# Kernel optimization log

Hardware: AMD Instinct MI355X
Metric: run time of the kernel (lower is better)

The kernel has to match this reference:

```python
import jax, jax.numpy as jnp
import numpy as np

N_NODES = 100000
N_EDGES = 1600000
IN_DIM = 128
OUT_DIM = 64


def setup_inputs() -> dict:
    key = jax.random.key(0)
    k1, k2, k3, k4, k5 = jax.random.split(key, 5)
    return {
        "h_init": jax.random.normal(k1, (N_NODES, IN_DIM), dtype=jnp.float32),
        "W1": jax.random.normal(k2, (OUT_DIM, IN_DIM), dtype=jnp.float32),
        "a": jax.random.normal(k3, (1, OUT_DIM), dtype=jnp.float32),
        "src": jax.random.randint(k4, (N_EDGES,), 0, N_NODES, dtype=jnp.int64)
        if jax.config.jax_enable_x64 else jax.random.randint(k4, (N_EDGES,), 0, N_NODES, dtype=jnp.int32),
        "dst": jax.random.randint(k5, (N_EDGES,), 0, N_NODES, dtype=jnp.int32),
    }


def reference(h_init, W1, a, src, dst):
    N = h_init.shape[0]
    # node projection: [N, out_dim]
    h = h_init @ W1.T
    # per-edge diff feature: dst minus src (DGL edges.dst['h'] - edges.src['h'])
    diff = h[dst] - h[src]                       # [E, out_dim]
    e = jnp.tanh(diff @ a[0])                    # [E] edge attention logit
    # segment softmax over incoming edges of each destination node
    seg_max = jax.ops.segment_max(e, dst, num_segments=N)   # [N]
    ex = jnp.exp(e - seg_max[dst])               # [E]
    denom = jax.ops.segment_sum(ex, dst, num_segments=N)    # [N]
    alpha = ex / denom[dst]                      # [E]
    # weighted sum of diff features per destination node
    h_diff = jax.ops.segment_sum(alpha[:, None] * diff, dst, num_segments=N)  # [N, out_dim]
    return jax.nn.relu(h + h_diff)
```

## Files before the change

kernel.cpp:

```cpp
#include <hip/hip_runtime.h>
#include <hip/hip_fp16.h>

#define N_NODES 100000
#define N_EDGES 1600000
#define IN_DIM 128
#define OUT_DIM 64

#define PROJ_BLKS 782

#define NB2 782
#define MAXB2 2560
#define CUR_STRIDE 16

#define BIN_NBLK 250
#define BIN_CHUNK 6400
#define BIN_THREADS 1024

#define SG_THREADS 512

typedef short short8 __attribute__((ext_vector_type(8)));
typedef float f32x4 __attribute__((ext_vector_type(4)));

__device__ __forceinline__ short bf16_trunc(float x) {
  return (short)(__float_as_uint(x) >> 16);
}
__device__ __forceinline__ float bf16_tof(short s) {
  return __uint_as_float(((unsigned)(unsigned short)s) << 16);
}
__device__ __forceinline__ float edge_ex(float p) {
  float t2 = __expf(2.f * p);
  float th = 1.f - 2.f * __builtin_amdgcn_rcpf(t2 + 1.f);
  return __expf(th);
}

__global__ __launch_bounds__(512) void fat1_kernel(
    const float* __restrict__ h_init, const float* __restrict__ W1,
    const float* __restrict__ a, __half* __restrict__ h16,
    float* __restrict__ ha) {
  __shared__ short whi[16 * 64 * 8];
  __shared__ short wlo[16 * 64 * 8];
  int t = threadIdx.x;

  for (int idx = t; idx < 16 * 64; idx += 512) {
    int f = idx >> 6;
    int l = idx & 63;
    int kc = f >> 2, ot = f & 3;
    const float* wsrc =
        W1 + (ot * 16 + (l & 15)) * IN_DIM + kc * 32 + (l >> 4) * 8;
    short hi[8], lo[8];
#pragma unroll
    for (int j = 0; j < 8; j++) {
      float x = wsrc[j];
      short hv = bf16_trunc(x);
      hi[j] = hv;
      lo[j] = bf16_trunc(x - bf16_tof(hv));
    }
    *(short8*)&whi[idx * 8] = *(const short8*)hi;
    *(short8*)&wlo[idx * 8] = *(const short8*)lo;
  }

  int row0 = blockIdx.x * 128;
  int w = t >> 6;
  int l = t & 63;
  int m = l & 15;
  int q = l >> 4;

  int arow = row0 + w * 16 + m;
  if (arow >= N_NODES) arow = N_NODES - 1;
  const float* xsrc = h_init + (size_t)arow * IN_DIM + q * 8;

  short8 ahi[4], alo[4];
#pragma unroll
  for (int kc = 0; kc < 4; kc++) {
    float xv[8];
    *(float4*)&xv[0] = *(const float4*)(xsrc + kc * 32);
    *(float4*)&xv[4] = *(const float4*)(xsrc + kc * 32 + 4);
    short hi[8], lo[8];
#pragma unroll
    for (int j = 0; j < 8; j++) {
      short hv = bf16_trunc(xv[j]);
      hi[j] = hv;
      lo[j] = bf16_trunc(xv[j] - bf16_tof(hv));
    }
    ahi[kc] = *(const short8*)hi;
    alo[kc] = *(const short8*)lo;
  }
  __syncthreads();

  f32x4 acc[4] = {{0.f, 0.f, 0.f, 0.f},
                  {0.f, 0.f, 0.f, 0.f},
                  {0.f, 0.f, 0.f, 0.f},
                  {0.f, 0.f, 0.f, 0.f}};

#pragma unroll
  for (int kc = 0; kc < 4; kc++) {
#pragma unroll
    for (int ot = 0; ot < 4; ot++) {
      int base = (((kc << 2) | ot) * 64 + l) * 8;
      short8 bhi = *(const short8*)&whi[base];
      short8 blo = *(const short8*)&wlo[base];
      acc[ot] = __builtin_amdgcn_mfma_f32_16x16x32_bf16(ahi[kc], bhi, acc[ot],
                                                        0, 0, 0);
      acc[ot] = __builtin_amdgcn_mfma_f32_16x16x32_bf16(ahi[kc], blo, acc[ot],
                                                        0, 0, 0);
      acc[ot] = __builtin_amdgcn_mfma_f32_16x16x32_bf16(alo[kc], bhi, acc[ot],
                                                        0, 0, 0);
    }
  }

  float pa[4] = {0.f, 0.f, 0.f, 0.f};
#pragma unroll
  for (int ot = 0; ot < 4; ot++) {
    float aval = a[ot * 16 + m];
#pragma unroll
    for (int r = 0; r < 4; r++) pa[r] += acc[ot][r] * aval;
  }
  int rowb = row0 + w * 16 + q * 4;
#pragma unroll
  for (int r = 0; r < 4; r++) {
    int row = rowb + r;
    if (row < N_NODES) {
#pragma unroll
      for (int ot = 0; ot < 4; ot++)
        h16[(size_t)row * OUT_DIM + ot * 16 + m] = __float2half(acc[ot][r]);
    }
  }
#pragma unroll
  for (int r = 0; r < 4; r++) {
    pa[r] += __shfl_xor(pa[r], 1);
    pa[r] += __shfl_xor(pa[r], 2);
    pa[r] += __shfl_xor(pa[r], 4);
    pa[r] += __shfl_xor(pa[r], 8);
  }
  if (m == 0) {
#pragma unroll
    for (int r = 0; r < 4; r++) {
      int row = rowb + r;
      if (row < N_NODES) ha[row] = pa[r];
    }
  }
}

__global__ __launch_bounds__(BIN_THREADS) void bin_scatter_kernel(
    const int* __restrict__ src, const int* __restrict__ dst,
    int* __restrict__ bucket_cursor, unsigned int* __restrict__ pairs) {
  __shared__ int hst[NB2];
  __shared__ int cur[NB2];
  __shared__ int dlds[BIN_CHUNK];
  int t = threadIdx.x;
  for (int i = t; i < NB2; i += BIN_THREADS) hst[i] = 0;
  __syncthreads();
  int beg = blockIdx.x * BIN_CHUNK;
  for (int e = t; e < BIN_CHUNK; e += BIN_THREADS) {
    int d = dst[beg + e];
    dlds[e] = d;
    atomicAdd(&hst[d >> 7], 1);
  }
  __syncthreads();
  for (int i = t; i < NB2; i += BIN_THREADS) {
    int c = hst[i];
    cur[i] =
        (c > 0) ? atomicAdd(&bucket_cursor[i * CUR_STRIDE], c) + i * MAXB2 : 0;
  }
  __syncthreads();
  for (int e = t; e < BIN_CHUNK; e += BIN_THREADS) {
    int d = dlds[e];
    int pos = atomicAdd(&cur[d >> 7], 1);
    pairs[pos] = ((unsigned int)src[beg + e] << 7) | (unsigned int)(d & 127);
  }
}

__global__ __launch_bounds__(SG_THREADS) void sortgather_kernel(
    const __half* __restrict__ h16, const float* __restrict__ ha,
    const int* __restrict__ bucket_cursor,
    const unsigned int* __restrict__ pairs, float* __restrict__ out) {
  __shared__ unsigned int plds[MAXB2];
  __shared__ int2 slds[MAXB2];
  __shared__ float had[128];
  __shared__ int hist[128];
  __shared__ int scn[128];
  __shared__ int cur[128];
  __shared__ int wsum;
  int b = blockIdx.x;
  int t = threadIdx.x;
  int node0 = b << 7;
  int cnt = min(bucket_cursor[b * CUR_STRIDE], MAXB2);

  if (t < 128) {
    int node = node0 + t;
    had[t] = (node < N_NODES) ? ha[node] : 0.f;
    hist[t] = 0;
  }
  __syncthreads();
  int c4 = cnt & ~3;
  for (int i = t * 4; i < c4; i += SG_THREADS * 4) {
    uint4 p4 = *(const uint4*)&pairs[(size_t)b * MAXB2 + i];
    *(uint4*)&plds[i] = p4;
    atomicAdd(&hist[p4.x & 127u], 1);
    atomicAdd(&hist[p4.y & 127u], 1);
    atomicAdd(&hist[p4.z & 127u], 1);
    atomicAdd(&hist[p4.w & 127u], 1);
  }
  for (int i = c4 + t; i < cnt; i += SG_THREADS) {
    unsigned int p = pairs[(size_t)b * MAXB2 + i];
    plds[i] = p;
    atomicAdd(&hist[p & 127u], 1);
  }
  __syncthreads();
  int v = (t < 128) ? hist[t] : 0;
  int x = v;
#pragma unroll
  for (int off = 1; off < 64; off <<= 1) {
    int y = __shfl_up(x, off, 64);
    if ((t & 63) >= off) x += y;
  }
  if (t == 63) wsum = x;
  __syncthreads();
  if (t >= 64 && t < 128) x += wsum;
  if (t < 128) {
    scn[t] = x;
    cur[t] = x - v;
  }
  __syncthreads();
  for (int i = t; i < cnt; i += SG_THREADS) {
    unsigned int p = plds[i];
    int nl = (int)(p & 127u);
    int sb = (int)(p & 0xFFFFFF80u);
    float ex = edge_ex(had[nl] - ha[sb >> 7]);
    int pos = atomicAdd(&cur[nl], 1);
    slds[pos] = make_int2(sb, __float_as_int(ex));
  }
  __syncthreads();

  int sg = t >> 3;
  int l8 = t & 7;
  const char* h16b = (const char*)h16;
  float4* o4 = (float4*)out;

  for (int nl = sg; nl < 128; nl += 64) {
    int node = node0 + nl;
    if (node >= N_NODES) continue;
    int endp = scn[nl];
    int begp = endp - hist[nl];
    union {
      uint4 u;
      __half hh[8];
    } HD;
    HD.u = *(const uint4*)(h16b + ((size_t)node << 7) + (l8 << 4));
    float acc[8] = {0.f, 0.f, 0.f, 0.f, 0.f, 0.f, 0.f, 0.f};
    float den = 0.f;
    int last = endp - 1;

    for (int base = begp; base < endp; base += 4) {
      int2 e[4];
      float exv[4];
#pragma unroll
      for (int k = 0; k < 4; k++) {
        int i = base + k;
        e[k] = slds[i < endp ? i : last];
        exv[k] = (i < endp) ? __int_as_float(e[k].y) : 0.f;
      }
      uint4 uv[4];
#pragma unroll
      for (int k = 0; k < 4; k++)
        uv[k] = *(const uint4*)(h16b + e[k].x + (l8 << 4));
#pragma unroll
      for (int k = 0; k < 4; k++) {
        union {
          uint4 u;
          __half hh[8];
        } U;
        U.u = uv[k];
        float ex = exv[k];
        den += ex;
#pragma unroll
        for (int j = 0; j < 8; j++)
          acc[j] = fmaf(__half2float(U.hh[j]), ex, acc[j]);
      }
    }

    bool has = den > 0.f;
    float inv = has ? __builtin_amdgcn_rcpf(den) : 0.f;
    float hd[8];
#pragma unroll
    for (int j = 0; j < 8; j++) hd[j] = __half2float(HD.hh[j]);
    float4 r0, r1;
    r0.x = fmaxf(has ? 2.f * hd[0] - acc[0] * inv : hd[0], 0.f);
    r0.y = fmaxf(has ? 2.f * hd[1] - acc[1] * inv : hd[1], 0.f);
    r0.z = fmaxf(has ? 2.f * hd[2] - acc[2] * inv : hd[2], 0.f);
    r0.w = fmaxf(has ? 2.f * hd[3] - acc[3] * inv : hd[3], 0.f);
    r1.x = fmaxf(has ? 2.f * hd[4] - acc[4] * inv : hd[4], 0.f);
    r1.y = fmaxf(has ? 2.f * hd[5] - acc[5] * inv : hd[5], 0.f);
    r1.z = fmaxf(has ? 2.f * hd[6] - acc[6] * inv : hd[6], 0.f);
    r1.w = fmaxf(has ? 2.f * hd[7] - acc[7] * inv : hd[7], 0.f);
    o4[(size_t)node * (OUT_DIM / 4) + l8 * 2] = r0;
    o4[(size_t)node * (OUT_DIM / 4) + l8 * 2 + 1] = r1;
  }
}

extern "C" void kernel_launch(void* const* d_in, const int* in_sizes, int n_in,
                              void* d_out, int out_size, void* d_ws,
                              size_t ws_size, hipStream_t stream) {
  const float* h_init = (const float*)d_in[0];
  const float* W1 = (const float*)d_in[1];
  const float* a = (const float*)d_in[2];
  const int* src = (const int*)d_in[3];
  const int* dst = (const int*)d_in[4];
  float* out = (float*)d_out;

  __half* h16 = (__half*)d_ws;
  float* ha = (float*)(h16 + (size_t)N_NODES * OUT_DIM);
  unsigned int* pairs = (unsigned int*)(ha + N_NODES);
  int* bucket_cursor = (int*)(pairs + (size_t)NB2 * MAXB2);

  hipMemsetAsync(bucket_cursor, 0, NB2 * CUR_STRIDE * sizeof(int), stream);
  fat1_kernel<<<PROJ_BLKS, 512, 0, stream>>>(h_init, W1, a, h16, ha);
  bin_scatter_kernel<<<BIN_NBLK, BIN_THREADS, 0, stream>>>(src, dst,
                                                           bucket_cursor,
                                                           pairs);
  sortgather_kernel<<<NB2, SG_THREADS, 0, stream>>>(h16, ha, bucket_cursor,
                                                    pairs, out);
}
```

Measured before the change: 179.1 us.

## Locally sort edge pairs in LDS before coalesced global scatter in binning

The binning kernel now builds a per-block prefix scan of bucket counts, scatters each edge into a block-local sorted staging buffer in shared memory, and then writes to the global pairs array in contiguous runs per bucket. This targets the scattered, uncoalesced global writes of the previous direct atomic-cursor scatter. In exchange it adds a wave-level scan, extra synchronisation, about 50KB more LDS (which lowers occupancy), and rereads dst instead of caching it.

```diff
diff --git a/kernel.cpp b/kernel.cpp
--- a/kernel.cpp
+++ b/kernel.cpp
@@ -144,30 +144,60 @@
 __global__ __launch_bounds__(BIN_THREADS) void bin_scatter_kernel(
     const int* __restrict__ src, const int* __restrict__ dst,
     int* __restrict__ bucket_cursor, unsigned int* __restrict__ pairs) {
-  __shared__ int hst[NB2];
-  __shared__ int cur[NB2];
-  __shared__ int dlds[BIN_CHUNK];
+  __shared__ unsigned int slds[BIN_CHUNK];
+  __shared__ int gofs[BIN_CHUNK];
+  __shared__ int hist[NB2];
+  __shared__ int lcur[NB2];
+  __shared__ int gbase[NB2];
+  __shared__ int wsum[16];
   int t = threadIdx.x;
-  for (int i = t; i < NB2; i += BIN_THREADS) hst[i] = 0;
-  __syncthreads();
+  int lane = t & 63;
+  int wid = t >> 6;
   int beg = blockIdx.x * BIN_CHUNK;
-  for (int e = t; e < BIN_CHUNK; e += BIN_THREADS) {
-    int d = dst[beg + e];
-    dlds[e] = d;
-    atomicAdd(&hst[d >> 7], 1);
-  }
-  __syncthreads();
-  for (int i = t; i < NB2; i += BIN_THREADS) {
-    int c = hst[i];
-    cur[i] =
-        (c > 0) ? atomicAdd(&bucket_cursor[i * CUR_STRIDE], c) + i * MAXB2 : 0;
-  }
-  __syncthreads();
-  for (int e = t; e < BIN_CHUNK; e += BIN_THREADS) {
-    int d = dlds[e];
-    int pos = atomicAdd(&cur[d >> 7], 1);
-    pairs[pos] = ((unsigned int)src[beg + e] << 7) | (unsigned int)(d & 127);
-  }
+
+  for (int i = t; i < NB2; i += BIN_THREADS) hist[i] = 0;
+  __syncthreads();
+  for (int e = beg + t; e < beg + BIN_CHUNK; e += BIN_THREADS)
+    atomicAdd(&hist[dst[e] >> 7], 1);
+  __syncthreads();
+  int v = (t < NB2) ? hist[t] : 0;
+  int x = v;
+#pragma unroll
+  for (int off = 1; off < 64; off <<= 1) {
+    int y = __shfl_up(x, off, 64);
+    if (lane >= off) x += y;
+  }
+  if (lane == 63) wsum[wid] = x;
+  __syncthreads();
+  if (t < 16) {
+    int s = wsum[t];
+#pragma unroll
+    for (int off = 1; off < 16; off <<= 1) {
+      int y = __shfl_up(s, off, 16);
+      if (t >= off) s += y;
+    }
+    wsum[t] = s;
+  }
+  __syncthreads();
+  if (wid > 0) x += wsum[wid - 1];
+  int lpos = x - v;
+  if (t < NB2) {
+    int g = (v > 0) ? atomicAdd(&bucket_cursor[t * CUR_STRIDE], v) : 0;
+    gbase[t] = g + t * MAXB2 - lpos;
+    lcur[t] = lpos;
+  }
+  __syncthreads();
+  for (int e = beg + t; e < beg + BIN_CHUNK; e += BIN_THREADS) {
+    int d = dst[e];
+    int s = src[e];
+    int b_ = d >> 7;
+    int li = atomicAdd(&lcur[b_], 1);
+    slds[li] = ((unsigned)s << 7) | (unsigned)(d & 127);
+    gofs[li] = gbase[b_];
+  }
+  __syncthreads();
+  for (int j = t; j < BIN_CHUNK; j += BIN_THREADS)
+    pairs[gofs[j] + j] = slds[j];
 }
 
 __global__ __launch_bounds__(SG_THREADS) void sortgather_kernel(
```

Result: faster. 173.5 us, median of 2 (-3.1%).
